# Kernel tuning notes

Measured on AMD Instinct MI355X. Metric: run time of the kernel, lower is better.

Reference implementation:

```python
import math
import jax, jax.numpy as jnp
import numpy as np


def setup_inputs() -> dict:
    key = jax.random.key(0)
    k1, k2, k3, k4 = jax.random.split(key, 4)
    B, C, H, W = 8, 256, 128, 128
    norm_dim, K = 64, 3
    return {
        "fea": jax.random.normal(k1, (B, C, H, W), dtype=jnp.float32),
        "norm_feat": jax.random.normal(k2, (B, norm_dim, 1, 1), dtype=jnp.float32),
        "mod_w": jax.random.normal(k3, (C, norm_dim, 1, 1), dtype=jnp.float32),
        "mod_b": jnp.zeros((C,), dtype=jnp.float32),
        "weight": jax.random.normal(k4, (1, C, C, K, K), dtype=jnp.float32),
    }


def reference(fea, norm_feat, mod_w, mod_b, weight):
    B, C, H, W = fea.shape
    K = weight.shape[-1]
    scale = 1.0 / math.sqrt(C * K * K)
    # 1x1 modulation conv on (B, norm_dim, 1, 1) -> style (B, C)
    style = jnp.einsum('bdhw,cd->bc', norm_feat, mod_w[:, :, 0, 0]) + mod_b  # (B, C)
    # modulate: (1, C_out, C_in, K, K) * (B, 1, C_in, 1, 1)
    w = scale * weight * style[:, None, :, None, None]  # (B, C, C, K, K)
    demod = jax.lax.rsqrt(jnp.sum(w * w, axis=(2, 3, 4)) + 1e-8)  # (B, C)
    w = w * demod[:, :, None, None, None]
    # grouped-conv trick: groups=B, input (1, B*C, H, W), weight (B*C, C, K, K)
    w = w.reshape(B * C, C, K, K)
    x = fea.reshape(1, B * C, H, W)
    out = jax.lax.conv_general_dilated(
        x, w,
        window_strides=(1, 1),
        padding=[(K // 2, K // 2), (K // 2, K // 2)],
        dimension_numbers=('NCHW', 'OIHW', 'NCHW'),
        feature_group_count=B,
    )
    return out.reshape(B, C, H, W)
```

## Files before the change

kernel.cpp:

```cpp
#include <hip/hip_runtime.h>

typedef unsigned short u16;
typedef unsigned int u32;
typedef short s8v __attribute__((ext_vector_type(8)));
typedef float f16v __attribute__((ext_vector_type(16)));
typedef u32 u32x4 __attribute__((ext_vector_type(4)));

__device__ __forceinline__ u16 f2bf(float f) {
    u32 u = __float_as_uint(f);
    u += 0x7FFFu + ((u >> 16) & 1u);
    return (u16)(u >> 16);
}

__device__ __forceinline__ void async_load16(const u16* g, u16* l) {
    __builtin_amdgcn_global_load_lds(
        (const __attribute__((address_space(1))) u32*)g,
        (__attribute__((address_space(3))) u32*)l,
        16, 0, 0);
}

__global__ void style_kernel(const float* __restrict__ norm_feat,
                             const float* __restrict__ mod_w,
                             const float* __restrict__ mod_b,
                             float* __restrict__ style) {
    __shared__ float nf[64];
    __shared__ float mw[256][65];
    const int b = blockIdx.x;
    const int tid = threadIdx.x;

    if (tid < 64) nf[tid] = norm_feat[b * 64 + tid];
    #pragma unroll
    for (int i = 0; i < 64; ++i) {
        int idx = i * 256 + tid;
        mw[idx >> 6][idx & 63] = mod_w[idx];
    }
    __syncthreads();

    float s = mod_b[tid];
    #pragma unroll 8
    for (int d = 0; d < 64; ++d) s += nf[d] * mw[tid][d];
    style[b * 256 + tid] = s;
}

__global__ void modulate_kernel(const float* __restrict__ style,
                                const float* __restrict__ weight,
                                u16* __restrict__ Wmod) {
    const int co = blockIdx.x;
    const int b  = blockIdx.y;
    const int ci = threadIdx.x;

    __shared__ float red[256];

    const float s = style[b * 256 + ci];

    float w9[9];
    const float* wp = weight + ((size_t)co * 256 + ci) * 9;
    float sq = 0.f;
    #pragma unroll
    for (int t = 0; t < 9; ++t) { w9[t] = wp[t]; sq += w9[t] * w9[t]; }

    red[ci] = sq * s * s;
    __syncthreads();
    for (int off = 128; off > 0; off >>= 1) {
        if (ci < off) red[ci] += red[ci + off];
        __syncthreads();
    }
    const float scale = 1.0f / 48.0f;
    const float demod = rsqrtf(scale * scale * red[0] + 1e-8f);
    const float coef  = scale * s * demod;

    const size_t tile = (((size_t)b * 9 * 8 + (co >> 5)) * 16 + (ci >> 4)) * 512
                      + (size_t)((co & 31) + 32 * ((ci >> 3) & 1)) * 8 + (ci & 7);
    #pragma unroll
    for (int t = 0; t < 9; ++t) {
        Wmod[tile + (size_t)t * 65536] = f2bf(w9[t] * coef);
    }
}

__global__ __launch_bounds__(256) void transpose_kernel(const float* __restrict__ fea,
                                                        u16* __restrict__ feaT) {
    __shared__ float lds_t[64][132];
    const int y = blockIdx.x;
    const int b = blockIdx.y;
    const int tid = threadIdx.x;

    for (int c0 = 0; c0 < 256; c0 += 64) {
        #pragma unroll
        for (int r = 0; r < 8; ++r) {
            int i  = r * 256 + tid;
            int c  = i >> 5;
            int x4 = i & 31;
            float4 v = *(const float4*)&fea[(((size_t)(b * 256 + c0 + c)) * 128 + y) * 128 + x4 * 4];
            *(float4*)&lds_t[c][x4 * 4] = v;
        }
        __syncthreads();
        #pragma unroll
        for (int jj = 0; jj < 4; ++jj) {
            int p   = jj * 256 + tid;
            int x   = p & 127;
            int g   = p >> 7;
            int cb8 = g * 8;
            u32x4 wv;
            #pragma unroll
            for (int k = 0; k < 4; ++k) {
                float f0 = lds_t[cb8 + 2 * k][x];
                float f1 = lds_t[cb8 + 2 * k + 1][x];
                wv[k] = (u32)f2bf(f0) | ((u32)f2bf(f1) << 16);
            }
            int c  = c0 + cb8;
            int ch = c >> 4;
            int cg = (c >> 3) & 1;
            size_t off = (((((size_t)b * 128 + y) * 16 + ch) * 2 + cg) * 128 + x) * 8;
            *(u32x4*)&feaT[off] = wv;
        }
        __syncthreads();
    }
}

__global__ __launch_bounds__(256, 2) void conv_mfma(
        const u16* __restrict__ Wmod,
        const u16* __restrict__ feaT,
        float* __restrict__ out) {
    __shared__ u16 lds[2][6168];

    const int lin = blockIdx.x + 128 * blockIdx.y;
    const int nid = (lin & 7) * 128 + (lin >> 3);
    const int y   = nid & 127;
    const int b   = nid >> 7;

    const int tid  = threadIdx.x;
    const int lane = tid & 63;
    const int wave = tid >> 6;
    const int mw  = wave & 1;
    const int nw  = wave >> 1;
    const int l31 = lane & 31;
    const int l5  = lane >> 5;

    if (tid < 24) { lds[0][6144 + tid] = 0; lds[1][6144 + tid] = 0; }

    const int xb0 = nw * 64 + l31 - 1;
    int ofj0[3], ofj1[3], bq0[3], bq2[3];
    #pragma unroll
    for (int kh = 0; kh < 3; ++kh) {
        const int rowb = ((kh * 2 + l5) * 128) * 8;
        const bool rok = (kh == 0) ? (y > 0) : (kh == 2 ? (y < 127) : true);
        const int o0 = rowb + xb0 * 8;
        const int o1 = o0 + 256;
        ofj0[kh] = rok ? o0 : 6144;
        ofj1[kh] = rok ? o1 : 6144;
        bq0[kh]  = (rok && xb0 >= 0)       ? o0        : 6144;
        bq2[kh]  = (rok && xb0 + 34 < 128) ? (o1 + 16) : 6144;
    }

    const u16* Abase = Wmod + (size_t)b * 9 * 65536
                            + (size_t)(mw * 4) * 8192 + (size_t)lane * 8;

    auto loadA = [&](int t, int i, int ch) -> s8v {
        return *(const s8v*)(Abase + (size_t)t * 65536 + (size_t)i * 8192 + (size_t)ch * 512);
    };

    auto stage = [&](int buf, int ch) {
        u16* ldsb = &lds[buf][0];
        #pragma unroll
        for (int i = 0; i < 3; ++i) {
            int u  = wave + 4 * i;
            int r  = u >> 2;
            int cg = (u >> 1) & 1;
            int xq = u & 1;
            int gy = y - 1 + r;
            if ((unsigned)gy < 128u) {
                const u16* g = feaT +
                    (((((size_t)b * 128 + gy) * 16 + ch) * 2 + cg) * 128 + xq * 64) * 8
                    + (size_t)lane * 8;
                async_load16(g, ldsb + ((r * 2 + cg) * 128 + xq * 64) * 8);
            }
        }
    };

    f16v acc[4][2];
    #pragma unroll
    for (int i = 0; i < 4; ++i)
        #pragma unroll
        for (int j = 0; j < 2; ++j) acc[i][j] = (f16v)0.0f;

    s8v fr[3][4];

    stage(0, 0);
    #pragma unroll
    for (int g = 0; g < 3; ++g)
        #pragma unroll
        for (int i = 0; i < 4; ++i) fr[g][i] = loadA(g, i, 0);
    __syncthreads();

    #pragma unroll 1
    for (int ch = 0; ch < 16; ++ch) {
        const u16* basep = &lds[ch & 1][0];

        s8v bfrE[2], bfrO[2];
        {
            const u16* a0 = basep + bq0[0];
            const u16* a1 = basep + ofj1[0];
            bfrE[0] = *(const s8v*)a0;
            bfrE[1] = *(const s8v*)a1;
        }

        #pragma unroll
        for (int t = 0; t < 9; ++t) {
            const int kh1 = (t + 1) / 3, kw1 = (t + 1) % 3;

            if ((t & 1) == 0) {
                if (t < 8) {
                    const u16* a0 = (kw1 == 0) ? (basep + bq0[kh1]) : (basep + ofj0[kh1] + kw1 * 8);
                    const u16* a1 = (kw1 == 2) ? (basep + bq2[kh1]) : (basep + ofj1[kh1] + kw1 * 8);
                    bfrO[0] = *(const s8v*)a0;
                    bfrO[1] = *(const s8v*)a1;
                }
                __builtin_amdgcn_s_setprio(1);
                #pragma unroll
                for (int i = 0; i < 4; ++i)
                    #pragma unroll
                    for (int j = 0; j < 2; ++j)
                        acc[i][j] = __builtin_amdgcn_mfma_f32_32x32x16_bf16(
                            fr[t % 3][i], bfrE[j], acc[i][j], 0, 0, 0);
                __builtin_amdgcn_s_setprio(0);
            } else {
                const u16* a0 = (kw1 == 0) ? (basep + bq0[kh1]) : (basep + ofj0[kh1] + kw1 * 8);
                const u16* a1 = (kw1 == 2) ? (basep + bq2[kh1]) : (basep + ofj1[kh1] + kw1 * 8);
                bfrE[0] = *(const s8v*)a0;
                bfrE[1] = *(const s8v*)a1;
                __builtin_amdgcn_s_setprio(1);
                #pragma unroll
                for (int i = 0; i < 4; ++i)
                    #pragma unroll
                    for (int j = 0; j < 2; ++j)
                        acc[i][j] = __builtin_amdgcn_mfma_f32_32x32x16_bf16(
                            fr[t % 3][i], bfrO[j], acc[i][j], 0, 0, 0);
                __builtin_amdgcn_s_setprio(0);
            }

            if (t < 6) {
                #pragma unroll
                for (int i = 0; i < 4; ++i) fr[t % 3][i] = loadA(t + 3, i, ch);
            } else if (ch < 15) {
                #pragma unroll
                for (int i = 0; i < 4; ++i) fr[t % 3][i] = loadA(t - 6, i, ch + 1);
            }

            if (t == 3 && ch < 15) {
                __builtin_amdgcn_sched_barrier(0);
                stage((ch + 1) & 1, ch + 1);
                __builtin_amdgcn_sched_barrier(0);
            }
        }

        if (ch < 15) {
            asm volatile("s_waitcnt vmcnt(12)" ::: "memory");
            __builtin_amdgcn_sched_barrier(0);
            __builtin_amdgcn_s_barrier();
            __builtin_amdgcn_sched_barrier(0);
        }
    }

    const int x_base = nw * 64 + l31;
    #pragma unroll
    for (int i = 0; i < 4; ++i) {
        #pragma unroll
        for (int j = 0; j < 2; ++j) {
            #pragma unroll
            for (int reg = 0; reg < 16; ++reg) {
                int co = mw * 128 + i * 32 + (reg & 3) + 8 * (reg >> 2) + 4 * l5;
                out[(((size_t)(b * 256 + co) * 128 + y) * 128) + x_base + j * 32] = acc[i][j][reg];
            }
        }
    }
}

extern "C" void kernel_launch(void* const* d_in, const int* in_sizes, int n_in,
                              void* d_out, int out_size, void* d_ws, size_t ws_size,
                              hipStream_t stream) {
    const float* fea       = (const float*)d_in[0];
    const float* norm_feat = (const float*)d_in[1];
    const float* mod_w     = (const float*)d_in[2];
    const float* mod_b     = (const float*)d_in[3];
    const float* weight    = (const float*)d_in[4];
    float* out = (float*)d_out;

    u16* Wmod = (u16*)d_ws;
    u16* feaT = (u16*)((char*)d_ws + 9u * 1024u * 1024u);
    float* style = (float*)feaT;

    style_kernel<<<dim3(8), 256, 0, stream>>>(norm_feat, mod_w, mod_b, style);
    modulate_kernel<<<dim3(256, 8), 256, 0, stream>>>(style, weight, Wmod);
    transpose_kernel<<<dim3(128, 8), 256, 0, stream>>>(fea, feaT);
    conv_mfma<<<dim3(128, 8), 256, 0, stream>>>(Wmod, feaT, out);
}
```

Baseline: 381.7 us.

## Compute two output rows per conv block and split transpose over channel groups

New measurement: 371.9 us. 2.6% less time.

```diff
diff --git a/kernel.cpp b/kernel.cpp
--- a/kernel.cpp
+++ b/kernel.cpp
@@ -80,76 +80,74 @@
 __global__ __launch_bounds__(256) void transpose_kernel(const float* __restrict__ fea,
                                                         u16* __restrict__ feaT) {
     __shared__ float lds_t[64][132];
-    const int y = blockIdx.x;
-    const int b = blockIdx.y;
+    const int y  = blockIdx.x;
+    const int c0 = blockIdx.y * 64;
+    const int b  = blockIdx.z;
     const int tid = threadIdx.x;
 
-    for (int c0 = 0; c0 < 256; c0 += 64) {
-        #pragma unroll
-        for (int r = 0; r < 8; ++r) {
-            int i  = r * 256 + tid;
-            int c  = i >> 5;
-            int x4 = i & 31;
-            float4 v = *(const float4*)&fea[(((size_t)(b * 256 + c0 + c)) * 128 + y) * 128 + x4 * 4];
-            *(float4*)&lds_t[c][x4 * 4] = v;
-        }
-        __syncthreads();
-        #pragma unroll
-        for (int jj = 0; jj < 4; ++jj) {
-            int p   = jj * 256 + tid;
-            int x   = p & 127;
-            int g   = p >> 7;
-            int cb8 = g * 8;
-            u32x4 wv;
-            #pragma unroll
-            for (int k = 0; k < 4; ++k) {
-                float f0 = lds_t[cb8 + 2 * k][x];
-                float f1 = lds_t[cb8 + 2 * k + 1][x];
-                wv[k] = (u32)f2bf(f0) | ((u32)f2bf(f1) << 16);
-            }
-            int c  = c0 + cb8;
-            int ch = c >> 4;
-            int cg = (c >> 3) & 1;
-            size_t off = (((((size_t)b * 128 + y) * 16 + ch) * 2 + cg) * 128 + x) * 8;
-            *(u32x4*)&feaT[off] = wv;
-        }
-        __syncthreads();
-    }
-}
-
-__global__ __launch_bounds__(256, 2) void conv_mfma(
+    #pragma unroll
+    for (int r = 0; r < 8; ++r) {
+        int i  = r * 256 + tid;
+        int c  = i >> 5;
+        int x4 = i & 31;
+        float4 v = *(const float4*)&fea[(((size_t)(b * 256 + c0 + c)) * 128 + y) * 128 + x4 * 4];
+        *(float4*)&lds_t[c][x4 * 4] = v;
+    }
+    __syncthreads();
+    #pragma unroll
+    for (int jj = 0; jj < 4; ++jj) {
+        int p   = jj * 256 + tid;
+        int x   = p & 127;
+        int g   = p >> 7;
+        int cb8 = g * 8;
+        u32x4 wv;
+        #pragma unroll
+        for (int k = 0; k < 4; ++k) {
+            float f0 = lds_t[cb8 + 2 * k][x];
+            float f1 = lds_t[cb8 + 2 * k + 1][x];
+            wv[k] = (u32)f2bf(f0) | ((u32)f2bf(f1) << 16);
+        }
+        int c  = c0 + cb8;
+        int ch = c >> 4;
+        int cg = (c >> 3) & 1;
+        size_t off = (((((size_t)b * 128 + y) * 16 + ch) * 2 + cg) * 128 + x) * 8;
+        *(u32x4*)&feaT[off] = wv;
+    }
+}
+
+__global__ __launch_bounds__(256, 1) void conv_mfma(
         const u16* __restrict__ Wmod,
         const u16* __restrict__ feaT,
         float* __restrict__ out) {
-    __shared__ u16 lds[2][6168];
-
-    const int lin = blockIdx.x + 128 * blockIdx.y;
-    const int nid = (lin & 7) * 128 + (lin >> 3);
-    const int y   = nid & 127;
-    const int b   = nid >> 7;
+    __shared__ u16 lds[2][8208];
+
+    const int lin = blockIdx.x + 64 * blockIdx.y;
+    const int nid = (lin & 7) * 64 + (lin >> 3);
+    const int yp  = nid & 63;
+    const int b   = nid >> 6;
 
     const int tid  = threadIdx.x;
     const int lane = tid & 63;
     const int wave = tid >> 6;
-    const int mw  = wave & 1;
-    const int nw  = wave >> 1;
-    const int l31 = lane & 31;
-    const int l5  = lane >> 5;
-
-    if (tid < 24) { lds[0][6144 + tid] = 0; lds[1][6144 + tid] = 0; }
-
-    const int xb0 = nw * 64 + l31 - 1;
-    int ofj0[3], ofj1[3], bq0[3], bq2[3];
+    const int mw   = wave & 1;
+    const int ywv  = wave >> 1;
+    const int l31  = lane & 31;
+    const int l5   = lane >> 5;
+
+    const int yw_s   = __builtin_amdgcn_readfirstlane(ywv);
+    const int y_out_s = 2 * yp + yw_s;
+    const bool rokU[3] = { y_out_s > 0, true, y_out_s < 127 };
+
+    if (tid < 16) { lds[0][8192 + tid] = 0; lds[1][8192 + tid] = 0; }
+
+    int rb[3], bqL[3], bqR[3];
     #pragma unroll
     for (int kh = 0; kh < 3; ++kh) {
-        const int rowb = ((kh * 2 + l5) * 128) * 8;
-        const bool rok = (kh == 0) ? (y > 0) : (kh == 2 ? (y < 127) : true);
-        const int o0 = rowb + xb0 * 8;
-        const int o1 = o0 + 256;
-        ofj0[kh] = rok ? o0 : 6144;
-        ofj1[kh] = rok ? o1 : 6144;
-        bq0[kh]  = (rok && xb0 >= 0)       ? o0        : 6144;
-        bq2[kh]  = (rok && xb0 + 34 < 128) ? (o1 + 16) : 6144;
+        const int rr = ywv + kh;
+        const int o  = ((rr * 2 + l5) * 128 + (l31 - 1)) * 8;
+        rb[kh]  = o;
+        bqL[kh] = (l31 > 0)  ? o : 8192;
+        bqR[kh] = (l31 < 31) ? (o + 3 * 256 + 16) : 8192;
     }
 
     const u16* Abase = Wmod + (size_t)b * 9 * 65536
@@ -161,13 +159,11 @@
 
     auto stage = [&](int buf, int ch) {
         u16* ldsb = &lds[buf][0];
-        #pragma unroll
-        for (int i = 0; i < 3; ++i) {
-            int u  = wave + 4 * i;
-            int r  = u >> 2;
-            int cg = (u >> 1) & 1;
-            int xq = u & 1;
-            int gy = y - 1 + r;
+        const int cg = wave >> 1;
+        const int xq = wave & 1;
+        #pragma unroll
+        for (int r = 0; r < 4; ++r) {
+            int gy = 2 * yp - 1 + r;
             if ((unsigned)gy < 128u) {
                 const u16* g = feaT +
                     (((((size_t)b * 128 + gy) * 16 + ch) * 2 + cg) * 128 + xq * 64) * 8
@@ -177,11 +173,11 @@
         }
     };
 
-    f16v acc[4][2];
+    f16v acc[4][4];
     #pragma unroll
     for (int i = 0; i < 4; ++i)
         #pragma unroll
-        for (int j = 0; j < 2; ++j) acc[i][j] = (f16v)0.0f;
+        for (int j = 0; j < 4; ++j) acc[i][j] = (f16v)0.0f;
 
     s8v fr[3][4];
 
@@ -196,46 +192,57 @@
     for (int ch = 0; ch < 16; ++ch) {
         const u16* basep = &lds[ch & 1][0];
 
-        s8v bfrE[2], bfrO[2];
-        {
-            const u16* a0 = basep + bq0[0];
-            const u16* a1 = basep + ofj1[0];
-            bfrE[0] = *(const s8v*)a0;
-            bfrE[1] = *(const s8v*)a1;
-        }
+        auto readB = [&](int kh, int kw, int j) -> s8v {
+            const u16* p;
+            if (j == 0 && kw == 0)      p = basep + bqL[kh];
+            else if (j == 3 && kw == 2) p = basep + bqR[kh];
+            else                        p = basep + rb[kh] + (j * 256 + kw * 8);
+            return *(const s8v*)p;
+        };
+
+        s8v bfrE[4], bfrO[4];
+        #pragma unroll
+        for (int j = 0; j < 4; ++j) bfrE[j] = readB(0, 0, j);
 
         #pragma unroll
         for (int t = 0; t < 9; ++t) {
-            const int kh1 = (t + 1) / 3, kw1 = (t + 1) % 3;
+            const int kh = t / 3, kw = t % 3;
+            const int khn = (t + 1) / 3, kwn = (t + 1) % 3;
 
             if ((t & 1) == 0) {
                 if (t < 8) {
-                    const u16* a0 = (kw1 == 0) ? (basep + bq0[kh1]) : (basep + ofj0[kh1] + kw1 * 8);
-                    const u16* a1 = (kw1 == 2) ? (basep + bq2[kh1]) : (basep + ofj1[kh1] + kw1 * 8);
-                    bfrO[0] = *(const s8v*)a0;
-                    bfrO[1] = *(const s8v*)a1;
+                    #pragma unroll
+                    for (int j = 0; j < 4; ++j) bfrO[j] = readB(khn, kwn, j);
                 }
-                __builtin_amdgcn_s_setprio(1);
+                if (rokU[kh]) {
+                    __builtin_amdgcn_s_setprio(1);
+                    #pragma unroll
+                    for (int i = 0; i < 4; ++i)
+                        #pragma unroll
+                        for (int j = 0; j < 4; ++j)
+                            acc[i][j] = __builtin_amdgcn_mfma_f32_32x32x16_bf16(
+                                fr[t % 3][i], bfrE[j], acc[i][j], 0, 0, 0);
+                    __builtin_amdgcn_s_setprio(0);
+                }
+            } else {
                 #pragma unroll
-                for (int i = 0; i < 4; ++i)
+                for (int j = 0; j < 4; ++j) bfrE[j] = readB(khn, kwn, j);
+                if (rokU[kh]) {
+                    __builtin_amdgcn_s_setprio(1);
                     #pragma unroll
-                    for (int j = 0; j < 2; ++j)
-                        acc[i][j] = __builtin_amdgcn_mfma_f32_32x32x16_bf16(
-                            fr[t % 3][i], bfrE[j], acc[i][j], 0, 0, 0);
-                __builtin_amdgcn_s_setprio(0);
-            } else {
-                const u16* a0 = (kw1 == 0) ? (basep + bq0[kh1]) : (basep + ofj0[kh1] + kw1 * 8);
-                const u16* a1 = (kw1 == 2) ? (basep + bq2[kh1]) : (basep + ofj1[kh1] + kw1 * 8);
-                bfrE[0] = *(const s8v*)a0;
-                bfrE[1] = *(const s8v*)a1;
-                __builtin_amdgcn_s_setprio(1);
-                #pragma unroll
-                for (int i = 0; i < 4; ++i)
-                    #pragma unroll
-                    for (int j = 0; j < 2; ++j)
-                        acc[i][j] = __builtin_amdgcn_mfma_f32_32x32x16_bf16(
-                            fr[t % 3][i], bfrO[j], acc[i][j], 0, 0, 0);
-                __builtin_amdgcn_s_setprio(0);
+                    for (int i = 0; i < 4; ++i)
+                        #pragma unroll
+                        for (int j = 0; j < 4; ++j)
+                            acc[i][j] = __builtin_amdgcn_mfma_f32_32x32x16_bf16(
+                                fr[t % 3][i], bfrO[j], acc[i][j], 0, 0, 0);
+                    __builtin_amdgcn_s_setprio(0);
+                }
+            }
+
+            if (t == 3 && ch < 15) {
+                __builtin_amdgcn_sched_barrier(0);
+                stage((ch + 1) & 1, ch + 1);
+                __builtin_amdgcn_sched_barrier(0);
             }
 
             if (t < 6) {
@@ -245,12 +252,6 @@
                 #pragma unroll
                 for (int i = 0; i < 4; ++i) fr[t % 3][i] = loadA(t - 6, i, ch + 1);
             }
-
-            if (t == 3 && ch < 15) {
-                __builtin_amdgcn_sched_barrier(0);
-                stage((ch + 1) & 1, ch + 1);
-                __builtin_amdgcn_sched_barrier(0);
-            }
         }
 
         if (ch < 15) {
@@ -261,15 +262,16 @@
         }
     }
 
-    const int x_base = nw * 64 + l31;
+    const int y_out = 2 * yp + ywv;
     #pragma unroll
     for (int i = 0; i < 4; ++i) {
         #pragma unroll
-        for (int j = 0; j < 2; ++j) {
+        for (int j = 0; j < 4; ++j) {
             #pragma unroll
             for (int reg = 0; reg < 16; ++reg) {
                 int co = mw * 128 + i * 32 + (reg & 3) + 8 * (reg >> 2) + 4 * l5;
-                out[(((size_t)(b * 256 + co) * 128 + y) * 128) + x_base + j * 32] = acc[i][j][reg];
+                int x  = j * 32 + l31;
+                out[(((size_t)(b * 256 + co) * 128 + y_out) * 128) + x] = acc[i][j][reg];
             }
         }
     }
@@ -291,6 +293,6 @@
 
     style_kernel<<<dim3(8), 256, 0, stream>>>(norm_feat, mod_w, mod_b, style);
     modulate_kernel<<<dim3(256, 8), 256, 0, stream>>>(style, weight, Wmod);
-    transpose_kernel<<<dim3(128, 8), 256, 0, stream>>>(fea, feaT);
-    conv_mfma<<<dim3(128, 8), 256, 0, stream>>>(Wmod, feaT, out);
-}
+    transpose_kernel<<<dim3(128, 4, 8), 256, 0, stream>>>(fea, feaT);
+    conv_mfma<<<dim3(64, 8), 256, 0, stream>>>(Wmod, feaT, out);
+}
```
